# Performance work log

Hardware: AMD Instinct MI355X
Metric: run time of the kernel (lower is better)

## Reference

```python
import jax, jax.numpy as jnp
import numpy as np

LN_EPS = 1e-5


def setup_inputs() -> dict:
    N, E, D = 50000, 800000, 128
    H = 4 * D
    key = jax.random.key(0)
    ks = jax.random.split(key, 8)
    h = jax.random.normal(ks[0], (N, D), dtype=jnp.float32)
    e_ij = jax.random.normal(ks[1], (E, D), dtype=jnp.float32)
    src = jax.random.randint(ks[2], (E,), 0, N, dtype=jnp.int32)
    dst = jax.random.randint(ks[3], (E,), 0, N, dtype=jnp.int32)
    # MLP params (torch nn.Linear default-style scale)
    W1 = jax.random.normal(ks[4], (D, H), dtype=jnp.float32) / np.sqrt(D)
    b1 = jnp.zeros((H,), dtype=jnp.float32)
    W2 = jax.random.normal(ks[5], (H, D), dtype=jnp.float32) / np.sqrt(H)
    b2 = jnp.zeros((D,), dtype=jnp.float32)
    gamma = jnp.ones((D,), dtype=jnp.float32)
    beta = jnp.zeros((D,), dtype=jnp.float32)
    return {"h": h, "e_ij": e_ij, "src": src, "dst": dst,
            "W1": W1, "b1": b1, "W2": W2, "b2": b2,
            "gamma": gamma, "beta": beta}


def reference(h, e_ij, src, dst, W1, b1, W2, b2, gamma, beta):
    N = h.shape[0]
    # update_all(copy_u('h'), sum): sum source-node features at each destination
    neigh = jax.ops.segment_sum(h[src], dst, num_segments=N)
    # update_all(copy_edge('e_ij'), sum): sum edge features at each destination
    u_edge = jax.ops.segment_sum(e_ij, dst, num_segments=N)
    u = neigh + u_edge                      # [N, D]
    # MLP: D -> 4D -> D with ReLU, then residual
    hid = jax.nn.relu(u @ W1 + b1)          # [N, 4D]
    out = hid @ W2 + b2 + h                 # [N, D]
    # LayerNorm over feature dim
    mean = jnp.mean(out, axis=-1, keepdims=True)
    var = jnp.var(out, axis=-1, keepdims=True)
    normed = (out - mean) * jax.lax.rsqrt(var + LN_EPS)
    # dropout with training=False is identity
    return normed * gamma + beta
```

## Files before the change

kernel.cpp:

```cpp
#include <hip/hip_runtime.h>

#define BM 64

typedef __bf16 bf16x8 __attribute__((ext_vector_type(8)));
typedef float f32x4 __attribute__((ext_vector_type(4)));
typedef float f4 __attribute__((ext_vector_type(4)));

__device__ __forceinline__ unsigned short f2bf(float x) {
  unsigned int u = __builtin_bit_cast(unsigned int, x);
  u += 0x7fffu + ((u >> 16) & 1u);
  return (unsigned short)(u >> 16);
}

__device__ __forceinline__ int swz(int row, int col) {
  return (row * 128 + col) ^ ((row & 7) << 3);
}

__device__ __forceinline__ f4 ntload4(const float* p) {
  return __builtin_nontemporal_load((const f4*)p);
}

__device__ __forceinline__ int wave_incl_scan(int v, int lane) {
  #pragma unroll
  for (int off = 1; off < 64; off <<= 1) {
    int t = __shfl_up(v, off, 64);
    if (lane >= off) v += t;
  }
  return v;
}

__global__ __launch_bounds__(256) void prep_weights(
    const float* __restrict__ W1, const float* __restrict__ W2,
    unsigned short* __restrict__ W1T, unsigned short* __restrict__ W2T,
    int* __restrict__ counts, int N) {
  int t = blockIdx.x * 256 + threadIdx.x;
  if (t < N) counts[t] = 0;
  {
    int hh = t >> 7, kk = t & 127;
    W1T[t] = f2bf(W1[kk * 512 + hh]);
  }
  {
    int dd = t >> 9, hh = t & 511;
    W2T[t] = f2bf(W2[hh * 128 + dd]);
  }
}

__global__ __launch_bounds__(256) void hist_dst(const int* __restrict__ dst,
                                                int* counts, int E) {
  int i = blockIdx.x * 256 + threadIdx.x;
  if (i < E) atomicAdd(&counts[dst[i]], 1);
}

__global__ __launch_bounds__(256) void scan1(const int* __restrict__ counts,
                                             int* offs, int* btot, int N) {
  int i = blockIdx.x * 256 + threadIdx.x;
  int lane = threadIdx.x & 63, wv = threadIdx.x >> 6;
  int v = (i < N) ? counts[i] : 0;
  int incl = wave_incl_scan(v, lane);
  __shared__ int wt[4];
  if (lane == 63) wt[wv] = incl;
  __syncthreads();
  int wpre = 0;
  for (int w = 0; w < wv; ++w) wpre += wt[w];
  if (i < N) offs[i] = wpre + incl - v;
  if (threadIdx.x == 255) btot[blockIdx.x] = wpre + incl;
}

__global__ __launch_bounds__(64) void scan2(int* btot, int nb) {
  int lane = threadIdx.x;
  __shared__ int carry_s;
  if (lane == 0) carry_s = 0;
  __syncthreads();
  for (int base = 0; base < nb; base += 64) {
    int i = base + lane;
    int v = (i < nb) ? btot[i] : 0;
    int incl = wave_incl_scan(v, lane);
    int carry = carry_s;
    if (i < nb) btot[i] = carry + incl - v;
    __syncthreads();
    if (lane == 63) carry_s = carry + incl;
    __syncthreads();
  }
}

__global__ __launch_bounds__(256) void scan3(int* offs, const int* __restrict__ btot,
                                             int N) {
  int i = blockIdx.x * 256 + threadIdx.x;
  if (i < N) offs[i] += btot[blockIdx.x];
}

__global__ __launch_bounds__(256) void build_perm(const int* __restrict__ dst,
                                                  int* offs, int* perm, int E) {
  int i = blockIdx.x * 256 + threadIdx.x;
  if (i < E) {
    int p = atomicAdd(&offs[dst[i]], 1);
    perm[p] = i;
  }
}

__global__ __launch_bounds__(256) void gather_sum(
    const float* __restrict__ hfeat, const float* __restrict__ eij,
    const int* __restrict__ src, const int* __restrict__ perm,
    const int* __restrict__ offs, const int* __restrict__ counts,
    float* __restrict__ u, int N) {
  int node = blockIdx.x * 4 + (threadIdx.x >> 6);
  if (node >= N) return;
  int lane = threadIdx.x & 63;
  int half = lane >> 5, c4 = (lane & 31) * 4;
  int cnt = counts[node];
  int beg = offs[node] - cnt;
  f4 acc = (f4){0.f, 0.f, 0.f, 0.f};
  int i = half;
  for (; i + 2 < cnt; i += 4) {
    int e0 = perm[beg + i];
    int e1 = perm[beg + i + 2];
    int s0 = src[e0], s1 = src[e1];
    f4 ev0 = ntload4(eij + (size_t)e0 * 128 + c4);
    f4 hv0 = *(const f4*)(hfeat + (size_t)s0 * 128 + c4);
    f4 ev1 = ntload4(eij + (size_t)e1 * 128 + c4);
    f4 hv1 = *(const f4*)(hfeat + (size_t)s1 * 128 + c4);
    acc += (ev0 + hv0) + (ev1 + hv1);
  }
  if (i < cnt) {
    int e = perm[beg + i];
    int s = src[e];
    f4 ev = ntload4(eij + (size_t)e * 128 + c4);
    f4 hv = *(const f4*)(hfeat + (size_t)s * 128 + c4);
    acc += ev + hv;
  }
  acc.x += __shfl_xor(acc.x, 32, 64);
  acc.y += __shfl_xor(acc.y, 32, 64);
  acc.z += __shfl_xor(acc.z, 32, 64);
  acc.w += __shfl_xor(acc.w, 32, 64);
  if (half == 0) *(f4*)(u + (size_t)node * 128 + c4) = acc;
}

__global__ __launch_bounds__(256, 2) void fused_mlp_ln(
    float* uo, const float* __restrict__ hfeat,
    const unsigned short* __restrict__ W1T, const unsigned short* __restrict__ W2T,
    const float* __restrict__ b1, const float* __restrict__ b2,
    const float* __restrict__ gma, const float* __restrict__ bta, int N) {
  __shared__ unsigned short As[BM * 128];
  __shared__ unsigned short Hs[BM * 128];
  __shared__ unsigned short Bs[128 * 128];

  const int tid = threadIdx.x;
  const int wave = tid >> 6, lane = tid & 63;
  const int lo = lane & 15, hi = lane >> 4;
  const int bm0 = blockIdx.x * BM;
  const int arow = wave * 16 + lo;

  #pragma unroll
  for (int i = 0; i < 8; ++i) {
    int q = i * 256 + tid;
    int r = q >> 5, c4 = (q & 31) * 4;
    f4 v = (f4){0.f, 0.f, 0.f, 0.f};
    if (bm0 + r < N) v = *(const f4*)(uo + (size_t)(bm0 + r) * 128 + c4);
    uint2 bv;
    bv.x = (unsigned)f2bf(v.x) | ((unsigned)f2bf(v.y) << 16);
    bv.y = (unsigned)f2bf(v.z) | ((unsigned)f2bf(v.w) << 16);
    *(uint2*)(&As[swz(r, c4)]) = bv;
  }

  f32x4 acc2[8];
  #pragma unroll
  for (int n = 0; n < 8; ++n) acc2[n] = (f32x4){0.f, 0.f, 0.f, 0.f};

  for (int c = 0; c < 4; ++c) {
    __syncthreads();
    #pragma unroll
    for (int i = 0; i < 8; ++i) {
      int q = i * 256 + tid;
      int r = q >> 4, c8 = (q & 15) * 8;
      uint4 w = *(const uint4*)(W1T + ((size_t)(c * 128 + r) * 128 + c8));
      *(uint4*)(&Bs[swz(r, c8)]) = w;
    }
    __syncthreads();

    f32x4 acc1[8];
    #pragma unroll
    for (int n = 0; n < 8; ++n) acc1[n] = (f32x4){0.f, 0.f, 0.f, 0.f};
    #pragma unroll
    for (int kk = 0; kk < 4; ++kk) {
      bf16x8 a = *(const bf16x8*)(&As[swz(arow, kk * 32 + hi * 8)]);
      #pragma unroll
      for (int n = 0; n < 8; ++n) {
        bf16x8 b = *(const bf16x8*)(&Bs[swz(n * 16 + lo, kk * 32 + hi * 8)]);
        acc1[n] = __builtin_amdgcn_mfma_f32_16x16x32_bf16(a, b, acc1[n], 0, 0, 0);
      }
    }
    #pragma unroll
    for (int n = 0; n < 8; ++n) {
      float bb = b1[c * 128 + n * 16 + lo];
      #pragma unroll
      for (int j = 0; j < 4; ++j) {
        float v = acc1[n][j] + bb;
        v = v > 0.f ? v : 0.f;
        Hs[swz(wave * 16 + hi * 4 + j, n * 16 + lo)] = f2bf(v);
      }
    }
    __syncthreads();
    #pragma unroll
    for (int i = 0; i < 8; ++i) {
      int q = i * 256 + tid;
      int r = q >> 4, c8 = (q & 15) * 8;
      uint4 w = *(const uint4*)(W2T + ((size_t)r * 512 + c * 128 + c8));
      *(uint4*)(&Bs[swz(r, c8)]) = w;
    }
    __syncthreads();
    #pragma unroll
    for (int kk = 0; kk < 4; ++kk) {
      bf16x8 a = *(const bf16x8*)(&Hs[swz(arow, kk * 32 + hi * 8)]);
      #pragma unroll
      for (int n = 0; n < 8; ++n) {
        bf16x8 b = *(const bf16x8*)(&Bs[swz(n * 16 + lo, kk * 32 + hi * 8)]);
        acc2[n] = __builtin_amdgcn_mfma_f32_16x16x32_bf16(a, b, acc2[n], 0, 0, 0);
      }
    }
  }

  float b2v[8], gv[8], bv2[8];
  #pragma unroll
  for (int n = 0; n < 8; ++n) {
    int d = n * 16 + lo;
    b2v[n] = b2[d]; gv[n] = gma[d]; bv2[n] = bta[d];
  }
  #pragma unroll
  for (int j = 0; j < 4; ++j) {
    int m = wave * 16 + hi * 4 + j;
    int grow = bm0 + m;
    bool valid = grow < N;
    float vals[8];
    float s = 0.f, s2 = 0.f;
    #pragma unroll
    for (int n = 0; n < 8; ++n) {
      float hres = valid ? hfeat[(size_t)grow * 128 + n * 16 + lo] : 0.f;
      float v = acc2[n][j] + b2v[n] + hres;
      vals[n] = v;
      s += v; s2 += v * v;
    }
    #pragma unroll
    for (int mk = 1; mk < 16; mk <<= 1) {
      s  += __shfl_xor(s, mk, 64);
      s2 += __shfl_xor(s2, mk, 64);
    }
    float mean = s * (1.f / 128.f);
    float var = s2 * (1.f / 128.f) - mean * mean;
    float inv = rsqrtf(var + 1e-5f);
    if (valid) {
      #pragma unroll
      for (int n = 0; n < 8; ++n) {
        uo[(size_t)grow * 128 + n * 16 + lo] = (vals[n] - mean) * inv * gv[n] + bv2[n];
      }
    }
  }
}

extern "C" void kernel_launch(void* const* d_in, const int* in_sizes, int n_in,
                              void* d_out, int out_size, void* d_ws, size_t ws_size,
                              hipStream_t stream) {
  (void)n_in; (void)out_size; (void)ws_size;
  const float* hfeat = (const float*)d_in[0];
  const float* eij   = (const float*)d_in[1];
  const int*   src   = (const int*)d_in[2];
  const int*   dst   = (const int*)d_in[3];
  const float* W1    = (const float*)d_in[4];
  const float* b1    = (const float*)d_in[5];
  const float* W2    = (const float*)d_in[6];
  const float* b2    = (const float*)d_in[7];
  const float* gma   = (const float*)d_in[8];
  const float* bta   = (const float*)d_in[9];
  float* out = (float*)d_out;

  int N = in_sizes[0] / 128;
  int E = in_sizes[2];
  int nb1 = (N + 255) / 256;

  char* ws = (char*)d_ws;
  unsigned short* W1T = (unsigned short*)ws;              ws += 512 * 128 * 2;
  unsigned short* W2T = (unsigned short*)ws;              ws += 128 * 512 * 2;
  int* counts = (int*)ws;                                 ws += (size_t)N * 4;
  int* offs   = (int*)ws;                                 ws += (size_t)N * 4;
  int* btot   = (int*)ws;                                 ws += ((nb1 + 63) / 64) * 64 * 4;
  int* perm   = (int*)ws;                                 ws += (size_t)E * 4;

  prep_weights<<<256, 256, 0, stream>>>(W1, W2, W1T, W2T, counts, N);
  hist_dst<<<(E + 255) / 256, 256, 0, stream>>>(dst, counts, E);
  scan1<<<nb1, 256, 0, stream>>>(counts, offs, btot, N);
  scan2<<<1, 64, 0, stream>>>(btot, nb1);
  scan3<<<nb1, 256, 0, stream>>>(offs, btot, N);
  build_perm<<<(E + 255) / 256, 256, 0, stream>>>(dst, offs, perm, E);

  gather_sum<<<(N + 3) / 4, 256, 0, stream>>>(hfeat, eij, src, perm, offs, counts,
                                              out, N);

  fused_mlp_ln<<<(N + BM - 1) / BM, 256, 0, stream>>>(out, hfeat, W1T, W2T,
                                                      b1, b2, gma, bta, N);
}
```

Baseline: 277.2 us.

## Pack edge id and source into perm, wave-load indices and shuffle

build_perm now stores (edge, src) pairs so gather_sum no longer needs a dependent src[e] lookup. gather_sum loads up to 64 index pairs with one coalesced wave-wide load and hands them out via __shfl. The main loop is unrolled to four edges per half-wave, keeping more independent feature loads in flight. The cost is a larger perm buffer (8 bytes per edge), an extra src read in build_perm, and more shuffle instructions.

```diff
diff --git a/kernel.cpp b/kernel.cpp
--- a/kernel.cpp
+++ b/kernel.cpp
@@ -90,17 +90,18 @@
 }
 
 __global__ __launch_bounds__(256) void build_perm(const int* __restrict__ dst,
-                                                  int* offs, int* perm, int E) {
+                                                  const int* __restrict__ src,
+                                                  int* offs, int2* perm2, int E) {
   int i = blockIdx.x * 256 + threadIdx.x;
   if (i < E) {
     int p = atomicAdd(&offs[dst[i]], 1);
-    perm[p] = i;
+    perm2[p] = make_int2(i, src[i]);
   }
 }
 
 __global__ __launch_bounds__(256) void gather_sum(
     const float* __restrict__ hfeat, const float* __restrict__ eij,
-    const int* __restrict__ src, const int* __restrict__ perm,
+    const int2* __restrict__ perm2,
     const int* __restrict__ offs, const int* __restrict__ counts,
     float* __restrict__ u, int N) {
   int node = blockIdx.x * 4 + (threadIdx.x >> 6);
@@ -110,23 +111,35 @@
   int cnt = counts[node];
   int beg = offs[node] - cnt;
   f4 acc = (f4){0.f, 0.f, 0.f, 0.f};
-  int i = half;
-  for (; i + 2 < cnt; i += 4) {
-    int e0 = perm[beg + i];
-    int e1 = perm[beg + i + 2];
-    int s0 = src[e0], s1 = src[e1];
-    f4 ev0 = ntload4(eij + (size_t)e0 * 128 + c4);
-    f4 hv0 = *(const f4*)(hfeat + (size_t)s0 * 128 + c4);
-    f4 ev1 = ntload4(eij + (size_t)e1 * 128 + c4);
-    f4 hv1 = *(const f4*)(hfeat + (size_t)s1 * 128 + c4);
-    acc += (ev0 + hv0) + (ev1 + hv1);
-  }
-  if (i < cnt) {
-    int e = perm[beg + i];
-    int s = src[e];
-    f4 ev = ntload4(eij + (size_t)e * 128 + c4);
-    f4 hv = *(const f4*)(hfeat + (size_t)s * 128 + c4);
-    acc += ev + hv;
+  for (int base = 0; base < cnt; base += 64) {
+    int m = cnt - base; if (m > 64) m = 64;
+    int2 es = perm2[beg + base + (lane < m ? lane : m - 1)];
+    int k = 0;
+    for (; 2 * k + 8 <= m; k += 4) {
+      int i0 = 2 * k + half;
+      int e0 = __shfl(es.x, i0, 64),     s0 = __shfl(es.y, i0, 64);
+      int e1 = __shfl(es.x, i0 + 2, 64), s1 = __shfl(es.y, i0 + 2, 64);
+      int e2 = __shfl(es.x, i0 + 4, 64), s2 = __shfl(es.y, i0 + 4, 64);
+      int e3 = __shfl(es.x, i0 + 6, 64), s3 = __shfl(es.y, i0 + 6, 64);
+      f4 ev0 = ntload4(eij + (size_t)e0 * 128 + c4);
+      f4 ev1 = ntload4(eij + (size_t)e1 * 128 + c4);
+      f4 ev2 = ntload4(eij + (size_t)e2 * 128 + c4);
+      f4 ev3 = ntload4(eij + (size_t)e3 * 128 + c4);
+      f4 hv0 = *(const f4*)(hfeat + (size_t)s0 * 128 + c4);
+      f4 hv1 = *(const f4*)(hfeat + (size_t)s1 * 128 + c4);
+      f4 hv2 = *(const f4*)(hfeat + (size_t)s2 * 128 + c4);
+      f4 hv3 = *(const f4*)(hfeat + (size_t)s3 * 128 + c4);
+      acc += (ev0 + hv0) + (ev1 + hv1) + (ev2 + hv2) + (ev3 + hv3);
+    }
+    for (; 2 * k < m; ++k) {
+      int idx = 2 * k + half;
+      int e = __shfl(es.x, idx & 63, 64), s = __shfl(es.y, idx & 63, 64);
+      if (idx < m) {
+        f4 ev = ntload4(eij + (size_t)e * 128 + c4);
+        f4 hv = *(const f4*)(hfeat + (size_t)s * 128 + c4);
+        acc += ev + hv;
+      }
+    }
   }
   acc.x += __shfl_xor(acc.x, 32, 64);
   acc.y += __shfl_xor(acc.y, 32, 64);
@@ -282,16 +295,17 @@
   int* counts = (int*)ws;                                 ws += (size_t)N * 4;
   int* offs   = (int*)ws;                                 ws += (size_t)N * 4;
   int* btot   = (int*)ws;                                 ws += ((nb1 + 63) / 64) * 64 * 4;
-  int* perm   = (int*)ws;                                 ws += (size_t)E * 4;
+  ws = (char*)(((uintptr_t)ws + 255) & ~(uintptr_t)255);
+  int2* perm2 = (int2*)ws;                                ws += (size_t)E * 8;
 
   prep_weights<<<256, 256, 0, stream>>>(W1, W2, W1T, W2T, counts, N);
   hist_dst<<<(E + 255) / 256, 256, 0, stream>>>(dst, counts, E);
   scan1<<<nb1, 256, 0, stream>>>(counts, offs, btot, N);
   scan2<<<1, 64, 0, stream>>>(btot, nb1);
   scan3<<<nb1, 256, 0, stream>>>(offs, btot, N);
-  build_perm<<<(E + 255) / 256, 256, 0, stream>>>(dst, offs, perm, E);
-
-  gather_sum<<<(N + 3) / 4, 256, 0, stream>>>(hfeat, eij, src, perm, offs, counts,
+  build_perm<<<(E + 255) / 256, 256, 0, stream>>>(dst, src, offs, perm2, E);
+
+  gather_sum<<<(N + 3) / 4, 256, 0, stream>>>(hfeat, eij, perm2, offs, counts,
                                               out, N);
 
   fused_mlp_ln<<<(N + BM - 1) / BM, 256, 0, stream>>>(out, hfeat, W1T, W2T,
```

After: 264.5 us. 4.6% less time.
